# Kernel optimization log

Hardware: AMD Instinct MI355X
Metric: run time of the kernel (lower is better)

Reference implementation:

```python
import jax, jax.numpy as jnp
import numpy as np

TEMPERATURE = 0.2
EPS = 1e-12  # matches torch F.normalize eps


def _l2_normalize(x):
    n = jnp.linalg.norm(x, axis=-1, keepdims=True)
    return x / jnp.maximum(n, EPS)


def setup_inputs() -> dict:
    key = jax.random.key(0)
    k1, k2 = jax.random.split(key)
    B, D = 8192, 256
    return {
        "user_embeddings": jax.random.normal(k1, (B, D), dtype=jnp.float32),
        "positive_item_embeddings": jax.random.normal(k2, (B, D), dtype=jnp.float32),
    }


def reference(user_embeddings, positive_item_embeddings):
    # all_item_embeddings=None branch: in-batch implicit negatives.
    u = _l2_normalize(user_embeddings)            # [B, D]
    p = _l2_normalize(positive_item_embeddings)   # [B, D]
    sim = jnp.einsum("bd,nd->bn", u, p) / TEMPERATURE  # [B, B]
    pos_sim = jnp.diagonal(sim)                   # [B]; equals the torch pos_sim
    # Original concatenates pos_sim[i] with the off-diagonal row entries and takes
    # logsumexp. Since the diagonal of sim IS pos_sim[i], that set equals the full
    # row, so loss_i = -pos_sim_i + logsumexp(sim[i, :]). Vectorized over the batch.
    lse = jax.nn.logsumexp(sim, axis=1)           # [B]
    return jnp.mean(lse - pos_sim)
```

## Files before the change

### kernel.cpp

```cpp
#include <hip/hip_runtime.h>
#include <hip/hip_bf16.h>

#define DDIM 256
#define NROWS 8192

typedef __attribute__((ext_vector_type(8))) __bf16 bf16x8;
typedef __attribute__((ext_vector_type(4))) float floatx4;

__device__ __forceinline__ void async16(const void* g, void* l) {
    __builtin_amdgcn_global_load_lds(
        (const __attribute__((address_space(1))) unsigned int*)g,
        (__attribute__((address_space(3))) unsigned int*)l,
        16, 0, 0);
}

__device__ __forceinline__ void stage_rows(const unsigned short* __restrict__ g,
                                           unsigned short* l,
                                           int wv, int lane,
                                           int rows_per_wave, int ninstr)
{
    const int lrow = lane >> 5;
    const int gcol = lane & 31;
    const int r0 = wv * rows_per_wave;
    for (int j = 0; j < ninstr; ++j) {
        const int rb = r0 + j * 2;
        const int r  = rb + lrow;
        const int gg = gcol ^ (r & 7);
        async16(g + (size_t)r * DDIM + gg * 8, l + (size_t)rb * DDIM);
    }
}

__device__ __forceinline__ bf16x8 frag(const unsigned short* base, int row,
                                       int ks, int q, int m)
{
    return *(const bf16x8*)&base[(size_t)row * DDIM
                                 + (((ks * 4 + q) ^ (m & 7)) * 8)];
}

__global__ __launch_bounds__(256) void normalize_kernel(
    const float* __restrict__ U, const float* __restrict__ P,
    unsigned short* __restrict__ Un, unsigned short* __restrict__ Pn,
    float* __restrict__ possim, float* __restrict__ rowsum,
    float* __restrict__ out, int* __restrict__ counter)
{
    if (blockIdx.x == 0 && threadIdx.x == 0) { out[0] = 0.0f; counter[0] = 0; }
    const int lane = threadIdx.x & 63;
    const int row  = blockIdx.x * 4 + (threadIdx.x >> 6);
    const size_t base = (size_t)row * DDIM + lane * 4;
    const float4 u4 = *(const float4*)(U + base);
    const float4 p4 = *(const float4*)(P + base);
    float su = u4.x*u4.x + u4.y*u4.y + u4.z*u4.z + u4.w*u4.w;
    float sp = p4.x*p4.x + p4.y*p4.y + p4.z*p4.z + p4.w*p4.w;
    float up = u4.x*p4.x + u4.y*p4.y + u4.z*p4.z + u4.w*p4.w;
    #pragma unroll
    for (int d = 1; d < 64; d <<= 1) {
        su += __shfl_xor(su, d);
        sp += __shfl_xor(sp, d);
        up += __shfl_xor(up, d);
    }
    const float iu = rsqrtf(fmaxf(su, 1e-24f));
    const float ip = rsqrtf(fmaxf(sp, 1e-24f));
    if (lane == 0) {
        possim[row] = up * iu * ip;
        rowsum[row] = 0.0f;
    }
    union { ushort4 s4; __hip_bfloat16 h[4]; } cu, cp;
    cu.h[0] = __float2bfloat16(u4.x * iu); cu.h[1] = __float2bfloat16(u4.y * iu);
    cu.h[2] = __float2bfloat16(u4.z * iu); cu.h[3] = __float2bfloat16(u4.w * iu);
    cp.h[0] = __float2bfloat16(p4.x * ip); cp.h[1] = __float2bfloat16(p4.y * ip);
    cp.h[2] = __float2bfloat16(p4.z * ip); cp.h[3] = __float2bfloat16(p4.w * ip);
    *(ushort4*)(Un + base) = cu.s4;
    *(ushort4*)(Pn + base) = cp.s4;
}

__global__ __launch_bounds__(256, 2) void sim_exp_rowsum(
    const unsigned short* __restrict__ Un,
    const unsigned short* __restrict__ Pn,
    float* __restrict__ rowsum,
    const float* __restrict__ possim,
    int* __restrict__ counter,
    float* __restrict__ out)
{
    __shared__ __align__(16) unsigned short lds[32768];
    __shared__ float ws4[4];
    __shared__ int ticket_s;

    const int tid  = threadIdx.x;
    const int lane = tid & 63;
    const int wv   = tid >> 6;
    const int wr   = wv >> 1, wc = wv & 1;
    const int m = lane & 15;
    const int q = lane >> 4;

    const int stripe = blockIdx.x >> 3;
    const int oct    = blockIdx.x & 7;

    const unsigned short* Aglob = Un + (size_t)stripe * 128 * DDIM;
    stage_rows(Aglob, lds, wv, lane, 32, 16);
    __syncthreads();

    bf16x8 afr[4][8];
    #pragma unroll
    for (int t = 0; t < 4; ++t)
        #pragma unroll
        for (int ks = 0; ks < 8; ++ks)
            afr[t][ks] = frag(lds, wr * 64 + t * 16 + m, ks, q, m);
    __syncthreads();

    const unsigned short* Bglob = Pn + (size_t)(oct * 1024) * DDIM;
    float rowpart[4][4];
    #pragma unroll
    for (int t = 0; t < 4; ++t)
        #pragma unroll
        for (int r = 0; r < 4; ++r)
            rowpart[t][r] = 0.0f;

    stage_rows(Bglob, lds, wv, lane, 16, 8);

    for (int i = 0; i < 16; ++i) {
        __syncthreads();
        if (i < 15)
            stage_rows(Bglob + (size_t)(i + 1) * 64 * DDIM,
                       lds + ((i + 1) & 1) * 16384, wv, lane, 16, 8);
        const unsigned short* Bp = lds + (i & 1) * 16384;

        floatx4 acc[4][2];
        #pragma unroll
        for (int t = 0; t < 4; ++t) {
            acc[t][0] = {0.0f, 0.0f, 0.0f, 0.0f};
            acc[t][1] = {0.0f, 0.0f, 0.0f, 0.0f};
        }
        #pragma unroll
        for (int ks = 0; ks < 8; ++ks) {
            const bf16x8 b0 = frag(Bp, wc * 32 + m,      ks, q, m);
            const bf16x8 b1 = frag(Bp, wc * 32 + 16 + m, ks, q, m);
            #pragma unroll
            for (int t = 0; t < 4; ++t) {
                acc[t][0] = __builtin_amdgcn_mfma_f32_16x16x32_bf16(
                    afr[t][ks], b0, acc[t][0], 0, 0, 0);
                acc[t][1] = __builtin_amdgcn_mfma_f32_16x16x32_bf16(
                    afr[t][ks], b1, acc[t][1], 0, 0, 0);
            }
        }
        #pragma unroll
        for (int t = 0; t < 4; ++t)
            #pragma unroll
            for (int r = 0; r < 4; ++r)
                rowpart[t][r] += __expf(5.0f * acc[t][0][r])
                               + __expf(5.0f * acc[t][1][r]);
    }

    #pragma unroll
    for (int t = 0; t < 4; ++t) {
        #pragma unroll
        for (int r = 0; r < 4; ++r) {
            float s = rowpart[t][r];
            s += __shfl_xor(s, 1);
            s += __shfl_xor(s, 2);
            s += __shfl_xor(s, 4);
            s += __shfl_xor(s, 8);
            if (m == 0) {
                const int grow = stripe * 128 + wr * 64 + t * 16 + q * 4 + r;
                atomicAdd(&rowsum[grow], s);
            }
        }
    }

    __threadfence();
    __syncthreads();
    if (tid == 0)
        ticket_s = __hip_atomic_fetch_add(counter, 1, __ATOMIC_ACQ_REL,
                                          __HIP_MEMORY_SCOPE_AGENT);
    __syncthreads();
    if (ticket_s == 511) {
        float part = 0.0f;
        for (int i = tid; i < NROWS; i += 256) {
            const float rs = __hip_atomic_load(&rowsum[i], __ATOMIC_RELAXED,
                                               __HIP_MEMORY_SCOPE_AGENT);
            part += __logf(rs) - 5.0f * possim[i];
        }
        #pragma unroll
        for (int d = 1; d < 64; d <<= 1) part += __shfl_xor(part, d);
        if (lane == 0) ws4[wv] = part;
        __syncthreads();
        if (tid == 0)
            out[0] = (ws4[0] + ws4[1] + ws4[2] + ws4[3]) * (1.0f / (float)NROWS);
    }
}

extern "C" void kernel_launch(void* const* d_in, const int* in_sizes, int n_in,
                              void* d_out, int out_size, void* d_ws, size_t ws_size,
                              hipStream_t stream) {
    const float* U = (const float*)d_in[0];
    const float* P = (const float*)d_in[1];
    float* out = (float*)d_out;
    char* ws = (char*)d_ws;
    unsigned short* Un = (unsigned short*)ws;
    unsigned short* Pn = (unsigned short*)(ws + 4194304);
    float* rowsum = (float*)(ws + 8388608);
    float* possim = (float*)(ws + 8388608 + 32768);
    int* counter  = (int*)(ws + 8388608 + 65536);

    normalize_kernel<<<NROWS / 4, 256, 0, stream>>>(U, P, Un, Pn, possim, rowsum,
                                                    out, counter);
    sim_exp_rowsum<<<512, 256, 0, stream>>>(Un, Pn, rowsum, possim, counter, out);
}
```

Baseline: 145.8 us.

## Deepen B-tile pipeline to 4 LDS buffers with manual waitcnt and exp2

The sim kernel changes how warps split the tile: each of the four waves now owns 32 A rows and sweeps all 32 B columns of a 32-row B tile, instead of a 2x2 wave grid over 64-row tiles. B tiles are staged through a four-deep ring of LDS buffers, using precomputed swizzled offsets and explicit vmcnt waits in place of a plain __syncthreads double buffer. This is meant to hide global-to-LDS latency better. The exponential also becomes a raw v_exp_f32 with the scale folded into a single multiply. The cost is that each B fragment is reused by fewer MFMAs and there are twice as many barriers, and the hand-written waitcnt counts have to match the async load counts exactly.

```diff
diff --git a/kernel.cpp b/kernel.cpp
--- a/kernel.cpp
+++ b/kernel.cpp
@@ -12,6 +12,10 @@
         (const __attribute__((address_space(1))) unsigned int*)g,
         (__attribute__((address_space(3))) unsigned int*)l,
         16, 0, 0);
+}
+
+__device__ __forceinline__ float fexp2(float x) {
+    float r; asm("v_exp_f32 %0, %1" : "=v"(r) : "v"(x)); return r;
 }
 
 __device__ __forceinline__ void stage_rows(const unsigned short* __restrict__ g,
@@ -73,6 +77,53 @@
     *(ushort4*)(Pn + base) = cp.s4;
 }
 
+__device__ __forceinline__ void stage_tile(const unsigned short* __restrict__ Bglob,
+                                           const unsigned* boff,
+                                           unsigned short* lds,
+                                           int t, int buf, int wv)
+{
+    const char* src = (const char*)Bglob + (unsigned)t * 16384u;
+    char* dst = (char*)lds + buf * 16384 + wv * 4096;
+    #pragma unroll
+    for (int jj = 0; jj < 4; ++jj)
+        async16(src + boff[jj], dst + jj * 1024);
+}
+
+template<int J>
+__device__ __forceinline__ void compute_tile(const unsigned short* lds,
+        const unsigned (&bb)[2][2], const bf16x8 (&afr)[2][8],
+        float (&rowpart)[2][4])
+{
+    floatx4 acc[2][2];
+    #pragma unroll
+    for (int t = 0; t < 2; ++t) {
+        acc[t][0] = {0.0f, 0.0f, 0.0f, 0.0f};
+        acc[t][1] = {0.0f, 0.0f, 0.0f, 0.0f};
+    }
+    const char* base = (const char*)lds;
+    #pragma unroll
+    for (int ks = 0; ks < 8; ++ks) {
+        const bf16x8 b0 = *(const bf16x8*)(base + bb[0][ks & 1]
+                                           + (J * 16384 + (ks >> 1) * 128));
+        const bf16x8 b1 = *(const bf16x8*)(base + bb[1][ks & 1]
+                                           + (J * 16384 + (ks >> 1) * 128));
+        #pragma unroll
+        for (int t = 0; t < 2; ++t) {
+            acc[t][0] = __builtin_amdgcn_mfma_f32_16x16x32_bf16(
+                afr[t][ks], b0, acc[t][0], 0, 0, 0);
+            acc[t][1] = __builtin_amdgcn_mfma_f32_16x16x32_bf16(
+                afr[t][ks], b1, acc[t][1], 0, 0, 0);
+        }
+    }
+    #pragma unroll
+    for (int t = 0; t < 2; ++t)
+        #pragma unroll
+        for (int h = 0; h < 2; ++h)
+            #pragma unroll
+            for (int r = 0; r < 4; ++r)
+                rowpart[t][r] += fexp2(acc[t][h][r] * 7.2134752044448169f);
+}
+
 __global__ __launch_bounds__(256, 2) void sim_exp_rowsum(
     const unsigned short* __restrict__ Un,
     const unsigned short* __restrict__ Pn,
@@ -88,7 +139,6 @@
     const int tid  = threadIdx.x;
     const int lane = tid & 63;
     const int wv   = tid >> 6;
-    const int wr   = wv >> 1, wc = wv & 1;
     const int m = lane & 15;
     const int q = lane >> 4;
 
@@ -99,59 +149,64 @@
     stage_rows(Aglob, lds, wv, lane, 32, 16);
     __syncthreads();
 
-    bf16x8 afr[4][8];
-    #pragma unroll
-    for (int t = 0; t < 4; ++t)
+    bf16x8 afr[2][8];
+    #pragma unroll
+    for (int t = 0; t < 2; ++t)
         #pragma unroll
         for (int ks = 0; ks < 8; ++ks)
-            afr[t][ks] = frag(lds, wr * 64 + t * 16 + m, ks, q, m);
-    __syncthreads();
+            afr[t][ks] = frag(lds, wv * 32 + t * 16 + m, ks, q, m);
+    __syncthreads();
+
+    const int c10 = m & 3, c2 = (m >> 2) & 1;
+    unsigned bb[2][2];
+    #pragma unroll
+    for (int h = 0; h < 2; ++h)
+        #pragma unroll
+        for (int par = 0; par < 2; ++par)
+            bb[h][par] = (unsigned)((h * 16 + m) * 512
+                                    + ((q ^ c10) << 4) + ((par ^ c2) << 6));
+
+    const int lrow = lane >> 5, gcol = lane & 31;
+    unsigned boff[4];
+    #pragma unroll
+    for (int jj = 0; jj < 4; ++jj) {
+        const int r = wv * 8 + jj * 2 + lrow;
+        const int gg = gcol ^ (r & 7);
+        boff[jj] = (unsigned)(r * 512 + gg * 16);
+    }
 
     const unsigned short* Bglob = Pn + (size_t)(oct * 1024) * DDIM;
-    float rowpart[4][4];
-    #pragma unroll
-    for (int t = 0; t < 4; ++t)
-        #pragma unroll
-        for (int r = 0; r < 4; ++r)
-            rowpart[t][r] = 0.0f;
-
-    stage_rows(Bglob, lds, wv, lane, 16, 8);
-
-    for (int i = 0; i < 16; ++i) {
-        __syncthreads();
-        if (i < 15)
-            stage_rows(Bglob + (size_t)(i + 1) * 64 * DDIM,
-                       lds + ((i + 1) & 1) * 16384, wv, lane, 16, 8);
-        const unsigned short* Bp = lds + (i & 1) * 16384;
-
-        floatx4 acc[4][2];
-        #pragma unroll
-        for (int t = 0; t < 4; ++t) {
-            acc[t][0] = {0.0f, 0.0f, 0.0f, 0.0f};
-            acc[t][1] = {0.0f, 0.0f, 0.0f, 0.0f};
-        }
-        #pragma unroll
-        for (int ks = 0; ks < 8; ++ks) {
-            const bf16x8 b0 = frag(Bp, wc * 32 + m,      ks, q, m);
-            const bf16x8 b1 = frag(Bp, wc * 32 + 16 + m, ks, q, m);
-            #pragma unroll
-            for (int t = 0; t < 4; ++t) {
-                acc[t][0] = __builtin_amdgcn_mfma_f32_16x16x32_bf16(
-                    afr[t][ks], b0, acc[t][0], 0, 0, 0);
-                acc[t][1] = __builtin_amdgcn_mfma_f32_16x16x32_bf16(
-                    afr[t][ks], b1, acc[t][1], 0, 0, 0);
-            }
-        }
-        #pragma unroll
-        for (int t = 0; t < 4; ++t)
-            #pragma unroll
-            for (int r = 0; r < 4; ++r)
-                rowpart[t][r] += __expf(5.0f * acc[t][0][r])
-                               + __expf(5.0f * acc[t][1][r]);
-    }
-
-    #pragma unroll
-    for (int t = 0; t < 4; ++t) {
+    float rowpart[2][4] = {{0.f, 0.f, 0.f, 0.f}, {0.f, 0.f, 0.f, 0.f}};
+
+    stage_tile(Bglob, boff, lds, 0, 0, wv);
+    stage_tile(Bglob, boff, lds, 1, 1, wv);
+    stage_tile(Bglob, boff, lds, 2, 2, wv);
+
+#define SLOT(JBUF, NWAIT, DOSTAGE, STAGET)                                   \
+    do {                                                                     \
+        asm volatile("s_waitcnt lgkmcnt(0)" ::: "memory");                   \
+        asm volatile("s_waitcnt vmcnt(" #NWAIT ")" ::: "memory");            \
+        __builtin_amdgcn_s_barrier();                                        \
+        if (DOSTAGE)                                                         \
+            stage_tile(Bglob, boff, lds, (STAGET), (STAGET) & 3, wv);        \
+        compute_tile<JBUF>(lds, bb, afr, rowpart);                           \
+    } while (0)
+
+    for (int i = 0; i < 7; ++i) {
+        const int t0 = i * 4;
+        SLOT(0, 8, true, t0 + 3);
+        SLOT(1, 8, true, t0 + 4);
+        SLOT(2, 8, true, t0 + 5);
+        SLOT(3, 8, true, t0 + 6);
+    }
+    SLOT(0, 8, true, 31);
+    SLOT(1, 8, false, 0);
+    SLOT(2, 4, false, 0);
+    SLOT(3, 0, false, 0);
+#undef SLOT
+
+    #pragma unroll
+    for (int t = 0; t < 2; ++t) {
         #pragma unroll
         for (int r = 0; r < 4; ++r) {
             float s = rowpart[t][r];
@@ -160,7 +215,7 @@
             s += __shfl_xor(s, 4);
             s += __shfl_xor(s, 8);
             if (m == 0) {
-                const int grow = stripe * 128 + wr * 64 + t * 16 + q * 4 + r;
+                const int grow = stripe * 128 + wv * 32 + t * 16 + q * 4 + r;
                 atomicAdd(&rowsum[grow], s);
             }
         }
```

Result: slower. 149.1 us (+2.3%).

## Retile sim kernel to 512-thread blocks with direct A loads and exp2

Applied to the files above, without the earlier changes.

The similarity/exp kernel now runs 8 waves per block. Each wave owns 32 rows of a 256-row stripe and loads its A fragments straight from global memory, with no LDS staging. Each block covers 512 columns in 8 steps of 64, with a changed LDS addressing pattern for B, and exp is computed through a raw v_exp_f32 on a prescaled argument. The intent is fewer registers per wave, higher occupancy, cheaper exponentials and less A staging, at the cost of B LDS traffic shared across more waves. There is some risk in the new swizzle and addressing being consistent with the staging layout.

```diff
diff --git a/kernel.cpp b/kernel.cpp
--- a/kernel.cpp
+++ b/kernel.cpp
@@ -14,27 +14,8 @@
         16, 0, 0);
 }
 
-__device__ __forceinline__ void stage_rows(const unsigned short* __restrict__ g,
-                                           unsigned short* l,
-                                           int wv, int lane,
-                                           int rows_per_wave, int ninstr)
-{
-    const int lrow = lane >> 5;
-    const int gcol = lane & 31;
-    const int r0 = wv * rows_per_wave;
-    for (int j = 0; j < ninstr; ++j) {
-        const int rb = r0 + j * 2;
-        const int r  = rb + lrow;
-        const int gg = gcol ^ (r & 7);
-        async16(g + (size_t)r * DDIM + gg * 8, l + (size_t)rb * DDIM);
-    }
-}
-
-__device__ __forceinline__ bf16x8 frag(const unsigned short* base, int row,
-                                       int ks, int q, int m)
-{
-    return *(const bf16x8*)&base[(size_t)row * DDIM
-                                 + (((ks * 4 + q) ^ (m & 7)) * 8)];
+__device__ __forceinline__ float fexp2(float x) {
+    float r; asm("v_exp_f32 %0, %1" : "=v"(r) : "v"(x)); return r;
 }
 
 __global__ __launch_bounds__(256) void normalize_kernel(
@@ -73,7 +54,24 @@
     *(ushort4*)(Pn + base) = cp.s4;
 }
 
-__global__ __launch_bounds__(256, 2) void sim_exp_rowsum(
+__device__ __forceinline__ void stage_rows(const unsigned short* __restrict__ g,
+                                           unsigned short* l,
+                                           int wv, int lane,
+                                           int rows_per_wave, int ninstr)
+{
+    const int lrow = lane >> 5;
+    const int gcol = lane & 31;
+    const int r0 = wv * rows_per_wave;
+    #pragma unroll
+    for (int j = 0; j < 4; ++j) {
+        const int rb = r0 + j * 2;
+        const int r  = rb + lrow;
+        const int gg = gcol ^ (r & 7);
+        async16(g + (size_t)r * DDIM + gg * 8, l + (size_t)rb * DDIM);
+    }
+}
+
+__global__ __launch_bounds__(512, 4) void sim_exp_rowsum(
     const unsigned short* __restrict__ Un,
     const unsigned short* __restrict__ Pn,
     float* __restrict__ rowsum,
@@ -82,76 +80,78 @@
     float* __restrict__ out)
 {
     __shared__ __align__(16) unsigned short lds[32768];
-    __shared__ float ws4[4];
+    __shared__ float ws8[8];
     __shared__ int ticket_s;
 
     const int tid  = threadIdx.x;
     const int lane = tid & 63;
     const int wv   = tid >> 6;
-    const int wr   = wv >> 1, wc = wv & 1;
     const int m = lane & 15;
     const int q = lane >> 4;
 
-    const int stripe = blockIdx.x >> 3;
-    const int oct    = blockIdx.x & 7;
-
-    const unsigned short* Aglob = Un + (size_t)stripe * 128 * DDIM;
-    stage_rows(Aglob, lds, wv, lane, 32, 16);
-    __syncthreads();
-
-    bf16x8 afr[4][8];
-    #pragma unroll
-    for (int t = 0; t < 4; ++t)
+    const int stripe = blockIdx.x >> 4;
+    const int cg     = blockIdx.x & 15;
+
+    const unsigned short* Arow = Un + (size_t)(stripe * 256 + wv * 32 + m) * DDIM;
+    bf16x8 afr[2][8];
+    #pragma unroll
+    for (int t = 0; t < 2; ++t)
         #pragma unroll
         for (int ks = 0; ks < 8; ++ks)
-            afr[t][ks] = frag(lds, wr * 64 + t * 16 + m, ks, q, m);
-    __syncthreads();
-
-    const unsigned short* Bglob = Pn + (size_t)(oct * 1024) * DDIM;
-    float rowpart[4][4];
-    #pragma unroll
-    for (int t = 0; t < 4; ++t)
-        #pragma unroll
-        for (int r = 0; r < 4; ++r)
-            rowpart[t][r] = 0.0f;
-
-    stage_rows(Bglob, lds, wv, lane, 16, 8);
-
-    for (int i = 0; i < 16; ++i) {
+            afr[t][ks] = *(const bf16x8*)(Arow + t * 16 * DDIM + (ks * 4 + q) * 8);
+
+    const int c10 = m & 3, c2 = (m >> 2) & 1;
+    unsigned bbp[2];
+    #pragma unroll
+    for (int par = 0; par < 2; ++par)
+        bbp[par] = (unsigned)(m * 512 + ((q ^ c10) << 4) + ((par ^ c2) << 6));
+
+    const unsigned short* Bglob = Pn + (size_t)(cg * 512) * DDIM;
+    float rowpart[2][4] = {{0.f, 0.f, 0.f, 0.f}, {0.f, 0.f, 0.f, 0.f}};
+
+    stage_rows(Bglob, lds, wv, lane, 8, 4);
+
+    for (int i = 0; i < 8; ++i) {
         __syncthreads();
-        if (i < 15)
+        if (i < 7)
             stage_rows(Bglob + (size_t)(i + 1) * 64 * DDIM,
-                       lds + ((i + 1) & 1) * 16384, wv, lane, 16, 8);
-        const unsigned short* Bp = lds + (i & 1) * 16384;
-
-        floatx4 acc[4][2];
-        #pragma unroll
-        for (int t = 0; t < 4; ++t) {
-            acc[t][0] = {0.0f, 0.0f, 0.0f, 0.0f};
-            acc[t][1] = {0.0f, 0.0f, 0.0f, 0.0f};
-        }
-        #pragma unroll
-        for (int ks = 0; ks < 8; ++ks) {
-            const bf16x8 b0 = frag(Bp, wc * 32 + m,      ks, q, m);
-            const bf16x8 b1 = frag(Bp, wc * 32 + 16 + m, ks, q, m);
-            #pragma unroll
-            for (int t = 0; t < 4; ++t) {
-                acc[t][0] = __builtin_amdgcn_mfma_f32_16x16x32_bf16(
-                    afr[t][ks], b0, acc[t][0], 0, 0, 0);
-                acc[t][1] = __builtin_amdgcn_mfma_f32_16x16x32_bf16(
-                    afr[t][ks], b1, acc[t][1], 0, 0, 0);
+                       lds + ((i + 1) & 1) * 16384, wv, lane, 8, 4);
+        const char* Bp = (const char*)(lds + (i & 1) * 16384);
+
+        #pragma unroll
+        for (int hh = 0; hh < 2; ++hh) {
+            floatx4 acc[2][2];
+            #pragma unroll
+            for (int t = 0; t < 2; ++t) {
+                acc[t][0] = {0.0f, 0.0f, 0.0f, 0.0f};
+                acc[t][1] = {0.0f, 0.0f, 0.0f, 0.0f};
             }
-        }
-        #pragma unroll
-        for (int t = 0; t < 4; ++t)
-            #pragma unroll
-            for (int r = 0; r < 4; ++r)
-                rowpart[t][r] += __expf(5.0f * acc[t][0][r])
-                               + __expf(5.0f * acc[t][1][r]);
-    }
-
-    #pragma unroll
-    for (int t = 0; t < 4; ++t) {
+            #pragma unroll
+            for (int ks = 0; ks < 8; ++ks) {
+                const bf16x8 b0 = *(const bf16x8*)(Bp + bbp[ks & 1]
+                        + ((hh * 2 + 0) * 8192 + (ks >> 1) * 128));
+                const bf16x8 b1 = *(const bf16x8*)(Bp + bbp[ks & 1]
+                        + ((hh * 2 + 1) * 8192 + (ks >> 1) * 128));
+                #pragma unroll
+                for (int t = 0; t < 2; ++t) {
+                    acc[t][0] = __builtin_amdgcn_mfma_f32_16x16x32_bf16(
+                        afr[t][ks], b0, acc[t][0], 0, 0, 0);
+                    acc[t][1] = __builtin_amdgcn_mfma_f32_16x16x32_bf16(
+                        afr[t][ks], b1, acc[t][1], 0, 0, 0);
+                }
+            }
+            #pragma unroll
+            for (int t = 0; t < 2; ++t)
+                #pragma unroll
+                for (int h = 0; h < 2; ++h)
+                    #pragma unroll
+                    for (int r = 0; r < 4; ++r)
+                        rowpart[t][r] += fexp2(acc[t][h][r] * 7.2134752044448169f);
+        }
+    }
+
+    #pragma unroll
+    for (int t = 0; t < 2; ++t) {
         #pragma unroll
         for (int r = 0; r < 4; ++r) {
             float s = rowpart[t][r];
@@ -160,7 +160,7 @@
             s += __shfl_xor(s, 4);
             s += __shfl_xor(s, 8);
             if (m == 0) {
-                const int grow = stripe * 128 + wr * 64 + t * 16 + q * 4 + r;
+                const int grow = stripe * 256 + wv * 32 + t * 16 + q * 4 + r;
                 atomicAdd(&rowsum[grow], s);
             }
         }
@@ -174,17 +174,21 @@
     __syncthreads();
     if (ticket_s == 511) {
         float part = 0.0f;
-        for (int i = tid; i < NROWS; i += 256) {
+        for (int i = tid; i < NROWS; i += 512) {
             const float rs = __hip_atomic_load(&rowsum[i], __ATOMIC_RELAXED,
                                                __HIP_MEMORY_SCOPE_AGENT);
             part += __logf(rs) - 5.0f * possim[i];
         }
         #pragma unroll
         for (int d = 1; d < 64; d <<= 1) part += __shfl_xor(part, d);
-        if (lane == 0) ws4[wv] = part;
+        if (lane == 0) ws8[wv] = part;
         __syncthreads();
-        if (tid == 0)
-            out[0] = (ws4[0] + ws4[1] + ws4[2] + ws4[3]) * (1.0f / (float)NROWS);
+        if (tid == 0) {
+            float tot = 0.0f;
+            #pragma unroll
+            for (int w = 0; w < 8; ++w) tot += ws8[w];
+            out[0] = tot * (1.0f / (float)NROWS);
+        }
     }
 }
 
@@ -203,5 +207,5 @@
 
     normalize_kernel<<<NROWS / 4, 256, 0, stream>>>(U, P, Un, Pn, possim, rowsum,
                                                     out, counter);
-    sim_exp_rowsum<<<512, 256, 0, stream>>>(Un, Pn, rowsum, possim, counter, out);
-}
+    sim_exp_rowsum<<<512, 512, 0, stream>>>(Un, Pn, rowsum, possim, counter, out);
+}
```

Measured after the change: 169.2 us. 16.1% more time.
